# Kernel optimization log

Measured on AMD Instinct MI355X. Metric: run time of the kernel, lower is better.

The kernel has to match this reference:

```python
import jax, jax.numpy as jnp
import numpy as np

B, N, DIM, H, KVAL = 16, 1024, 128, 8, 4  # b divisible by K*K=16; mask batch = B//(K*K)=1


def setup_inputs() -> dict:
    key = jax.random.key(0)
    ks = jax.random.split(key, 6)
    x = jax.random.normal(ks[0], (B, N, DIM), jnp.float32)
    mask = (jax.random.uniform(ks[1], (B // (KVAL * KVAL), N - 1)) < 0.9).astype(jnp.float32)
    maps = (jax.random.uniform(ks[2], (B, N - 1)) < 0.9).astype(jnp.float32)
    Wqkv = jax.random.normal(ks[3], (DIM, 3 * DIM), jnp.float32) / np.sqrt(DIM)
    Wout = jax.random.normal(ks[4], (DIM, DIM), jnp.float32) / np.sqrt(DIM)
    bout = jnp.zeros((DIM,), jnp.float32)
    return {"x": x, "mask": mask, "maps": maps, "Wqkv": Wqkv, "Wout": Wout,
            "bout": bout, "K": KVAL}


def reference(x, mask, maps, Wqkv, Wout, bout, K):
    b, n, dim = x.shape
    h = H
    d = dim // h
    scale = dim ** -0.5
    qkv = x @ Wqkv                                  # [b, n, 3*dim]
    q, k, v = jnp.split(qkv, 3, axis=-1)

    def to_heads(t):
        return t.reshape(b, n, h, d).transpose(0, 2, 1, 3)  # [b, h, n, d]

    q, k, v = to_heads(q), to_heads(k), to_heads(v)
    dots = jnp.einsum('bhid,bhjd->bhij', q, k) * scale      # [b, h, n, n]
    mask_value = -jnp.finfo(dots.dtype).max

    # block mask: pad first key position with 1, broadcast over K*K batch block
    kk = K * K
    m = jnp.pad(mask, ((0, 0), (1, 0)), constant_values=1.0)  # [b//kk, n]
    dots = dots.reshape(b // kk, kk, h, n, n)
    m5 = m[:, None, None, None, :]
    dots = dots * m5 + mask_value * (1.0 - m5)
    dots = dots.reshape(b, h, n, n)

    # map mask: boolean fill per batch element
    mp = jnp.pad(maps, ((0, 0), (1, 0)), constant_values=1.0)  # [b, n]
    dots = jnp.where(mp[:, None, None, :] != 0, dots, mask_value)

    attn = jax.nn.softmax(dots, axis=-1)
    out = jnp.einsum('bhij,bhjd->bhid', attn, v)            # [b, h, n, d]
    out = out.transpose(0, 2, 1, 3).reshape(b, n, dim)      # [b, n, dim]
    return out @ Wout + bout
```

## Files before the change

### kernel.cpp

```cpp
#include <hip/hip_runtime.h>
#include <math.h>

#define B_   16
#define N_   1024
#define DIM_ 128
#define H_   8
#define D_   16
#define BH_  128

typedef unsigned short u16;
typedef unsigned int   u32;
typedef __attribute__((ext_vector_type(8))) short short8;
typedef __attribute__((ext_vector_type(4))) float f32x4;

__device__ __forceinline__ float bf2f(u16 u) {
    union { u32 i; float f; } c; c.i = ((u32)u) << 16; return c.f;
}
__device__ __forceinline__ u16 f2bf(float f) {
    union { float f; u32 i; } c; c.f = f;
    u32 r = c.i + 0x7FFFu + ((c.i >> 16) & 1u);
    return (u16)(r >> 16);
}
__device__ __forceinline__ u32 pack2bf(float a, float b) {
    union { float f; u32 i; } ca, cb; ca.f = a; cb.f = b;
    return ((ca.i + 0x8000u) >> 16) | ((cb.i + 0x8000u) & 0xFFFF0000u);
}
union frag8 { short8 s; u32 w[4]; };

#define BF_ONE  ((short)0x3F80)
#define BF_NINF ((u16)0xFF80)

#define SCALE_L2E (0.08838834764831845f * 1.4426950408889634f)

__global__ __launch_bounds__(256) void prep_kernel(
    const float* __restrict__ x, const float* __restrict__ Wqkv,
    const float* __restrict__ Wout,
    u16* __restrict__ xb, u16* __restrict__ wqkvb, u16* __restrict__ woutb)
{
    const int b = blockIdx.x, tid = threadIdx.x;
    if (b < 2048) {
        const int i = b * 256 + tid;
        float4 v = ((const float4*)x)[i];
        ushort4 o = make_ushort4(f2bf(v.x), f2bf(v.y), f2bf(v.z), f2bf(v.w));
        *(ushort4*)(xb + (size_t)i * 4) = o;
    } else {
        const int t = (b - 2048) * 256 + tid;
        if (t < 49152) {
            const int k = t / 384, col = t - k * 384;
            wqkvb[(size_t)col * 128 + k] = f2bf(Wqkv[t]);
        } else {
            const int t2 = t - 49152;
            const int k = t2 >> 7, col = t2 & 127;
            woutb[(size_t)col * 128 + k] = f2bf(Wout[t2]);
        }
    }
}

__global__ __launch_bounds__(256) void qkv_kernel(
    const u16* __restrict__ xb, const u16* __restrict__ wqkvb,
    const float* __restrict__ maskp, const float* __restrict__ mapsp,
    u16* __restrict__ qws, u16* __restrict__ kws2, u16* __restrict__ vtws)
{
    const int tid  = threadIdx.x;
    const int wave = tid >> 6, lane = tid & 63;
    const int i16  = lane & 15, quad = lane >> 4;
    const int cb   = blockIdx.x % 6;
    const int rb   = blockIdx.x / 6;
    const int row_m = rb * 64 + wave * 16;

    const u16* xp = xb + (size_t)(row_m + i16) * 128;
    const u16* wb = wqkvb + (size_t)(cb * 64 + i16) * 128;

    f32x4 acc0 = {0,0,0,0}, acc1 = {0,0,0,0}, acc2 = {0,0,0,0}, acc3 = {0,0,0,0};

    #pragma unroll
    for (int ks = 0; ks < 4; ks++) {
        const int k0 = ks * 32 + quad * 8;
        const short8 a = *(const short8*)(xp + k0);
        acc0 = __builtin_amdgcn_mfma_f32_16x16x32_bf16(
                   a, *(const short8*)(wb + k0), acc0, 0, 0, 0);
        acc1 = __builtin_amdgcn_mfma_f32_16x16x32_bf16(
                   a, *(const short8*)(wb + 16 * 128 + k0), acc1, 0, 0, 0);
        acc2 = __builtin_amdgcn_mfma_f32_16x16x32_bf16(
                   a, *(const short8*)(wb + 32 * 128 + k0), acc2, 0, 0, 0);
        acc3 = __builtin_amdgcn_mfma_f32_16x16x32_bf16(
                   a, *(const short8*)(wb + 48 * 128 + k0), acc3, 0, 0, 0);
    }

    const int which = (cb * 64) >> 7;
    const int row   = row_m + quad * 4;
    const int bb    = row >> 10, n = row & 1023;

    #define STORE_CT(CT, ACC) { \
        const int c  = (cb * 64 + CT * 16) & 127; \
        const int h  = c >> 4; \
        const int bh = bb * 8 + h; \
        const int dd = i16; \
        if (which == 0) { \
            u16* p = qws + ((size_t)(bh * N_ + n)) * 16 + dd; \
            p[0]  = f2bf(ACC[0] * SCALE_L2E); p[16] = f2bf(ACC[1] * SCALE_L2E); \
            p[32] = f2bf(ACC[2] * SCALE_L2E); p[48] = f2bf(ACC[3] * SCALE_L2E); \
        } else if (which == 1) { \
            u16* p = kws2 + ((size_t)(bh * N_ + n)) * 32 + dd; \
            p[0]  = f2bf(ACC[0]); p[32] = f2bf(ACC[1]); \
            p[64] = f2bf(ACC[2]); p[96] = f2bf(ACC[3]); \
            if (dd == 0) { \
                _Pragma("unroll") \
                for (int r = 0; r < 4; r++) { \
                    const int nr = n + r; \
                    const bool valid = (nr == 0) || \
                        (maskp[nr - 1] != 0.0f && mapsp[bb * (N_ - 1) + nr - 1] != 0.0f); \
                    kws2[((size_t)(bh * N_ + nr)) * 32 + 16] = valid ? (u16)0 : BF_NINF; \
                } \
            } \
        } else { \
            *(ushort4*)(vtws + ((size_t)(bh * 16 + dd)) * N_ + n) = \
                make_ushort4(f2bf(ACC[0]), f2bf(ACC[1]), f2bf(ACC[2]), f2bf(ACC[3])); \
        } }
    STORE_CT(0, acc0)
    STORE_CT(1, acc1)
    STORE_CT(2, acc2)
    STORE_CT(3, acc3)
    #undef STORE_CT
}

__global__ __launch_bounds__(256) void attn_kernel(
    const u16* __restrict__ qws, const u16* __restrict__ kws2, const u16* __restrict__ vtws,
    u16* __restrict__ attn)
{
    const int tid  = threadIdx.x;
    const int wave = tid >> 6, lane = tid & 63;
    const int i16  = lane & 15, quad = lane >> 4;
    const int bh   = blockIdx.x;
    const int qb   = blockIdx.y;
    const int bb   = bh >> 3, h = bh & 7;
    const int qrow0 = qb * 256 + wave * 64;
    const int perm = ((i16 & 12) << 1) | (i16 & 3);

    const short8 zero8 = {0,0,0,0,0,0,0,0};
    const short8 ones8 = {BF_ONE,BF_ONE,BF_ONE,BF_ONE,BF_ONE,BF_ONE,BF_ONE,BF_ONE};

    short8 qf0 = zero8, qf1 = zero8, qf2 = zero8, qf3 = zero8;
    if (lane < 32) {
        const u16* qp = qws + ((size_t)(bh * N_ + qrow0 + i16)) * 16 + quad * 8;
        qf0 = *(const short8*)(qp);
        qf1 = *(const short8*)(qp + 256);
        qf2 = *(const short8*)(qp + 512);
        qf3 = *(const short8*)(qp + 768);
    } else if (lane < 48) {
        qf0[0] = BF_ONE; qf1[0] = BF_ONE; qf2[0] = BF_ONE; qf3[0] = BF_ONE;
    }

    const u16* kpA = kws2 + ((size_t)(bh * N_ + perm)) * 32 + quad * 8;
    const u16* kpB = kpA + 4 * 32;
    const u16* vp  = vtws + ((size_t)(bh * 16 + i16)) * N_ + quad * 8;

    f32x4 o0 = {0,0,0,0}, o1 = {0,0,0,0}, o2 = {0,0,0,0}, o3 = {0,0,0,0};
    f32x4 l0 = {0,0,0,0}, l1 = {0,0,0,0}, l2 = {0,0,0,0}, l3 = {0,0,0,0};
    const f32x4 zc = {0.f, 0.f, 0.f, 0.f};

    #pragma unroll 2
    for (int j0 = 0; j0 < N_; j0 += 32) {
        const short8 kfA = *(const short8*)kpA;
        const short8 kfB = *(const short8*)kpB;
        const short8 vf  = *(const short8*)vp;
        kpA += 32 * 32; kpB += 32 * 32; vp += 32;

        #define TILE(QF, O, L) { \
            f32x4 stA = __builtin_amdgcn_mfma_f32_16x16x32_bf16(kfA, QF, zc, 0, 0, 0); \
            f32x4 stB = __builtin_amdgcn_mfma_f32_16x16x32_bf16(kfB, QF, zc, 0, 0, 0); \
            float pA0 = __builtin_amdgcn_exp2f(stA[0]); \
            float pA1 = __builtin_amdgcn_exp2f(stA[1]); \
            float pA2 = __builtin_amdgcn_exp2f(stA[2]); \
            float pA3 = __builtin_amdgcn_exp2f(stA[3]); \
            float pB0 = __builtin_amdgcn_exp2f(stB[0]); \
            float pB1 = __builtin_amdgcn_exp2f(stB[1]); \
            float pB2 = __builtin_amdgcn_exp2f(stB[2]); \
            float pB3 = __builtin_amdgcn_exp2f(stB[3]); \
            frag8 pk; \
            pk.w[0] = pack2bf(pA0, pA1); pk.w[1] = pack2bf(pA2, pA3); \
            pk.w[2] = pack2bf(pB0, pB1); pk.w[3] = pack2bf(pB2, pB3); \
            O = __builtin_amdgcn_mfma_f32_16x16x32_bf16(vf,    pk.s, O, 0, 0, 0); \
            L = __builtin_amdgcn_mfma_f32_16x16x32_bf16(ones8, pk.s, L, 0, 0, 0); \
        }
        TILE(qf0, o0, l0)
        TILE(qf1, o1, l1)
        TILE(qf2, o2, l2)
        TILE(qf3, o3, l3)
        #undef TILE
    }

    #define OUT_T(T, O, L) { \
        const float inv = 1.0f / L[0]; \
        ushort4 pko = make_ushort4(f2bf(O[0] * inv), f2bf(O[1] * inv), \
                                   f2bf(O[2] * inv), f2bf(O[3] * inv)); \
        *(ushort4*)(attn + ((size_t)(bb * N_ + qrow0 + T * 16 + i16)) * DIM_ \
                    + h * 16 + quad * 4) = pko; }
    OUT_T(0, o0, l0)
    OUT_T(1, o1, l1)
    OUT_T(2, o2, l2)
    OUT_T(3, o3, l3)
    #undef OUT_T
}

__global__ __launch_bounds__(256) void out_kernel(
    const u16* __restrict__ attnw, const u16* __restrict__ woutb,
    const float* __restrict__ boutp, float* __restrict__ outp)
{
    const int tid  = threadIdx.x;
    const int wave = tid >> 6, lane = tid & 63;
    const int i16  = lane & 15, quad = lane >> 4;
    const int cb   = blockIdx.x & 1;
    const int rb   = blockIdx.x >> 1;
    const int row_m = rb * 64 + wave * 16;

    const u16* ap = attnw + (size_t)(row_m + i16) * 128;
    const u16* wb = woutb + (size_t)(cb * 64 + i16) * 128;

    f32x4 acc0 = {0,0,0,0}, acc1 = {0,0,0,0}, acc2 = {0,0,0,0}, acc3 = {0,0,0,0};

    #pragma unroll
    for (int ks = 0; ks < 4; ks++) {
        const int k0 = ks * 32 + quad * 8;
        const short8 a = *(const short8*)(ap + k0);
        acc0 = __builtin_amdgcn_mfma_f32_16x16x32_bf16(
                   a, *(const short8*)(wb + k0), acc0, 0, 0, 0);
        acc1 = __builtin_amdgcn_mfma_f32_16x16x32_bf16(
                   a, *(const short8*)(wb + 16 * 128 + k0), acc1, 0, 0, 0);
        acc2 = __builtin_amdgcn_mfma_f32_16x16x32_bf16(
                   a, *(const short8*)(wb + 32 * 128 + k0), acc2, 0, 0, 0);
        acc3 = __builtin_amdgcn_mfma_f32_16x16x32_bf16(
                   a, *(const short8*)(wb + 48 * 128 + k0), acc3, 0, 0, 0);
    }

    const int row = row_m + quad * 4;
    #define STORE_CT(CT, ACC) { \
        const int col = cb * 64 + CT * 16 + i16; \
        const float bo = boutp[col]; \
        float* op = outp + (size_t)row * 128 + col; \
        op[0 * 128] = ACC[0] + bo; \
        op[1 * 128] = ACC[1] + bo; \
        op[2 * 128] = ACC[2] + bo; \
        op[3 * 128] = ACC[3] + bo; \
    }
    STORE_CT(0, acc0)
    STORE_CT(1, acc1)
    STORE_CT(2, acc2)
    STORE_CT(3, acc3)
    #undef STORE_CT
}

extern "C" void kernel_launch(void* const* d_in, const int* in_sizes, int n_in,
                              void* d_out, int out_size, void* d_ws, size_t ws_size,
                              hipStream_t stream) {
    const float* x    = (const float*)d_in[0];
    const float* mask = (const float*)d_in[1];
    const float* maps = (const float*)d_in[2];
    const float* Wqkv = (const float*)d_in[3];
    const float* Wout = (const float*)d_in[4];
    const float* bout = (const float*)d_in[5];
    u16* qws    = (u16*)d_ws;
    u16* kws2   = qws   + (size_t)2 * 1024 * 1024;
    u16* vtws   = kws2  + (size_t)4 * 1024 * 1024;
    u16* attn   = vtws  + (size_t)2 * 1024 * 1024;
    u16* xbws   = attn  + (size_t)2 * 1024 * 1024;
    u16* wqkvb  = xbws  + (size_t)2 * 1024 * 1024;
    u16* woutb  = wqkvb + (size_t)384 * 128;

    prep_kernel<<<dim3(2304), dim3(256), 0, stream>>>(x, Wqkv, Wout, xbws, wqkvb, woutb);
    qkv_kernel<<<dim3(1536), dim3(256), 0, stream>>>(xbws, wqkvb, mask, maps, qws, kws2, vtws);
    attn_kernel<<<dim3(128, 4), dim3(256), 0, stream>>>(qws, kws2, vtws, attn);
    out_kernel<<<dim3(512), dim3(256), 0, stream>>>(attn, woutb, bout, (float*)d_out);
}
```

Baseline: 134.9 us.

## Fuse all four stages into one cooperative kernel with grid syncs

Replaces the four separate launches (weight/x conversion, QKV projection, attention, output projection) with a single cooperative kernel of 512 blocks that uses grid.sync between stages. The QKV stage now converts x from fp32 to bf16 in registers instead of running a separate conversion pass, and each block covers three column tiles. This targets launch overhead and the round trip of writing and rereading bf16 x. In exchange the grid is fixed at 512 blocks for every stage, which lowers parallelism in the QKV stage, and the grid-wide barriers add cost. The old four-kernel path remains as a fallback if the cooperative launch fails.

```diff
diff --git a/kernel.cpp b/kernel.cpp
--- a/kernel.cpp
+++ b/kernel.cpp
@@ -1,5 +1,8 @@
 #include <hip/hip_runtime.h>
+#include <hip/hip_cooperative_groups.h>
 #include <math.h>
+
+namespace cg = cooperative_groups;
 
 #define B_   16
 #define N_   1024
@@ -29,8 +32,216 @@
 
 #define BF_ONE  ((short)0x3F80)
 #define BF_NINF ((u16)0xFF80)
-
 #define SCALE_L2E (0.08838834764831845f * 1.4426950408889634f)
+
+#define MFMA16 __builtin_amdgcn_mfma_f32_16x16x32_bf16
+
+__global__ __launch_bounds__(256) void fused_kernel(
+    const float* __restrict__ x, const float* __restrict__ maskp,
+    const float* __restrict__ mapsp, const float* __restrict__ Wqkv,
+    const float* __restrict__ Wout, const float* __restrict__ boutp,
+    u16* __restrict__ qws, u16* __restrict__ kws2, u16* __restrict__ vtws,
+    u16* __restrict__ attnw, u16* __restrict__ wqkvb, u16* __restrict__ woutb,
+    float* __restrict__ outp)
+{
+    cg::grid_group grid = cg::this_grid();
+    const int blk  = blockIdx.x;
+    const int tid  = threadIdx.x;
+    const int wave = tid >> 6, lane = tid & 63;
+    const int i16  = lane & 15, quad = lane >> 4;
+
+    {
+        const int t = blk * 256 + tid;
+        if (t < 49152) {
+            const int k = t / 384, col = t - k * 384;
+            wqkvb[(size_t)col * 128 + k] = f2bf(Wqkv[t]);
+        } else if (t < 65536) {
+            const int t2 = t - 49152;
+            const int k = t2 >> 7, col = t2 & 127;
+            woutb[(size_t)col * 128 + k] = f2bf(Wout[t2]);
+        }
+    }
+    grid.sync();
+
+    {
+        const int rb  = blk >> 1;
+        const int cb0 = (blk & 1) * 3;
+        const int row_m = rb * 64 + wave * 16;
+        const float* xp = x + (size_t)(row_m + i16) * 128;
+
+        short8 a0, a1, a2, a3;
+        #define LOADA(A, K0) { \
+            const int k0 = (K0) + quad * 8; \
+            const float4 xa = *(const float4*)(xp + k0); \
+            const float4 xb2 = *(const float4*)(xp + k0 + 4); \
+            frag8 t_; \
+            t_.w[0] = pack2bf(xa.x, xa.y); t_.w[1] = pack2bf(xa.z, xa.w); \
+            t_.w[2] = pack2bf(xb2.x, xb2.y); t_.w[3] = pack2bf(xb2.z, xb2.w); \
+            A = t_.s; }
+        LOADA(a0, 0) LOADA(a1, 32) LOADA(a2, 64) LOADA(a3, 96)
+        #undef LOADA
+
+        const int row = row_m + quad * 4;
+        const int bb  = row >> 10, n = row & 1023;
+
+        for (int ci = 0; ci < 3; ci++) {
+            const int cb = cb0 + ci;
+            const u16* wb = wqkvb + (size_t)(cb * 64 + i16) * 128;
+            f32x4 acc0 = {0,0,0,0}, acc1 = {0,0,0,0}, acc2 = {0,0,0,0}, acc3 = {0,0,0,0};
+            #define KSTEP(A, K0) { \
+                const int k0 = (K0) + quad * 8; \
+                acc0 = MFMA16(A, *(const short8*)(wb + k0),            acc0, 0,0,0); \
+                acc1 = MFMA16(A, *(const short8*)(wb + 16*128 + k0),   acc1, 0,0,0); \
+                acc2 = MFMA16(A, *(const short8*)(wb + 32*128 + k0),   acc2, 0,0,0); \
+                acc3 = MFMA16(A, *(const short8*)(wb + 48*128 + k0),   acc3, 0,0,0); }
+            KSTEP(a0, 0) KSTEP(a1, 32) KSTEP(a2, 64) KSTEP(a3, 96)
+            #undef KSTEP
+
+            const int which = (cb * 64) >> 7;
+            #define STORE_CT(CT, ACC) { \
+                const int c  = (cb * 64 + CT * 16) & 127; \
+                const int h  = c >> 4; \
+                const int bh = bb * 8 + h; \
+                const int dd = i16; \
+                if (which == 0) { \
+                    u16* p = qws + ((size_t)(bh * N_ + n)) * 16 + dd; \
+                    p[0]  = f2bf(ACC[0] * SCALE_L2E); p[16] = f2bf(ACC[1] * SCALE_L2E); \
+                    p[32] = f2bf(ACC[2] * SCALE_L2E); p[48] = f2bf(ACC[3] * SCALE_L2E); \
+                } else if (which == 1) { \
+                    u16* p = kws2 + ((size_t)(bh * N_ + n)) * 32 + dd; \
+                    p[0]  = f2bf(ACC[0]); p[32] = f2bf(ACC[1]); \
+                    p[64] = f2bf(ACC[2]); p[96] = f2bf(ACC[3]); \
+                    if (dd == 0) { \
+                        _Pragma("unroll") \
+                        for (int r = 0; r < 4; r++) { \
+                            const int nr = n + r; \
+                            const bool valid = (nr == 0) || \
+                                (maskp[nr - 1] != 0.0f && mapsp[bb * (N_ - 1) + nr - 1] != 0.0f); \
+                            kws2[((size_t)(bh * N_ + nr)) * 32 + 16] = valid ? (u16)0 : BF_NINF; \
+                        } \
+                    } \
+                } else { \
+                    *(ushort4*)(vtws + ((size_t)(bh * 16 + dd)) * N_ + n) = \
+                        make_ushort4(f2bf(ACC[0]), f2bf(ACC[1]), f2bf(ACC[2]), f2bf(ACC[3])); \
+                } }
+            STORE_CT(0, acc0)
+            STORE_CT(1, acc1)
+            STORE_CT(2, acc2)
+            STORE_CT(3, acc3)
+            #undef STORE_CT
+        }
+    }
+    grid.sync();
+
+    {
+        const int bh = blk >> 2;
+        const int qb = blk & 3;
+        const int bb = bh >> 3, h = bh & 7;
+        const int qrow0 = qb * 256 + wave * 64;
+        const int perm = ((i16 & 12) << 1) | (i16 & 3);
+
+        const short8 zero8 = {0,0,0,0,0,0,0,0};
+        const short8 ones8 = {BF_ONE,BF_ONE,BF_ONE,BF_ONE,BF_ONE,BF_ONE,BF_ONE,BF_ONE};
+
+        short8 qf0 = zero8, qf1 = zero8, qf2 = zero8, qf3 = zero8;
+        if (lane < 32) {
+            const u16* qp = qws + ((size_t)(bh * N_ + qrow0 + i16)) * 16 + quad * 8;
+            qf0 = *(const short8*)(qp);
+            qf1 = *(const short8*)(qp + 256);
+            qf2 = *(const short8*)(qp + 512);
+            qf3 = *(const short8*)(qp + 768);
+        } else if (lane < 48) {
+            qf0[0] = BF_ONE; qf1[0] = BF_ONE; qf2[0] = BF_ONE; qf3[0] = BF_ONE;
+        }
+
+        const u16* kpA = kws2 + ((size_t)(bh * N_ + perm)) * 32 + quad * 8;
+        const u16* kpB = kpA + 4 * 32;
+        const u16* vp  = vtws + ((size_t)(bh * 16 + i16)) * N_ + quad * 8;
+
+        f32x4 o0 = {0,0,0,0}, o1 = {0,0,0,0}, o2 = {0,0,0,0}, o3 = {0,0,0,0};
+        f32x4 l0 = {0,0,0,0}, l1 = {0,0,0,0}, l2 = {0,0,0,0}, l3 = {0,0,0,0};
+        const f32x4 zc = {0.f, 0.f, 0.f, 0.f};
+
+        #pragma unroll 2
+        for (int j0 = 0; j0 < N_; j0 += 32) {
+            const short8 kfA = *(const short8*)kpA;
+            const short8 kfB = *(const short8*)kpB;
+            const short8 vf  = *(const short8*)vp;
+            kpA += 32 * 32; kpB += 32 * 32; vp += 32;
+
+            #define TILE(QF, O, L) { \
+                f32x4 stA = MFMA16(kfA, QF, zc, 0, 0, 0); \
+                f32x4 stB = MFMA16(kfB, QF, zc, 0, 0, 0); \
+                float pA0 = __builtin_amdgcn_exp2f(stA[0]); \
+                float pA1 = __builtin_amdgcn_exp2f(stA[1]); \
+                float pA2 = __builtin_amdgcn_exp2f(stA[2]); \
+                float pA3 = __builtin_amdgcn_exp2f(stA[3]); \
+                float pB0 = __builtin_amdgcn_exp2f(stB[0]); \
+                float pB1 = __builtin_amdgcn_exp2f(stB[1]); \
+                float pB2 = __builtin_amdgcn_exp2f(stB[2]); \
+                float pB3 = __builtin_amdgcn_exp2f(stB[3]); \
+                frag8 pk; \
+                pk.w[0] = pack2bf(pA0, pA1); pk.w[1] = pack2bf(pA2, pA3); \
+                pk.w[2] = pack2bf(pB0, pB1); pk.w[3] = pack2bf(pB2, pB3); \
+                O = MFMA16(vf,    pk.s, O, 0, 0, 0); \
+                L = MFMA16(ones8, pk.s, L, 0, 0, 0); }
+            TILE(qf0, o0, l0)
+            TILE(qf1, o1, l1)
+            TILE(qf2, o2, l2)
+            TILE(qf3, o3, l3)
+            #undef TILE
+        }
+
+        #define OUT_T(T, O, L) { \
+            const float inv = 1.0f / L[0]; \
+            ushort4 pko = make_ushort4(f2bf(O[0] * inv), f2bf(O[1] * inv), \
+                                       f2bf(O[2] * inv), f2bf(O[3] * inv)); \
+            *(ushort4*)(attnw + ((size_t)(bb * N_ + qrow0 + T * 16 + i16)) * DIM_ \
+                        + h * 16 + quad * 4) = pko; }
+        OUT_T(0, o0, l0)
+        OUT_T(1, o1, l1)
+        OUT_T(2, o2, l2)
+        OUT_T(3, o3, l3)
+        #undef OUT_T
+    }
+    grid.sync();
+
+    {
+        const int cb = blk & 1;
+        const int rb = blk >> 1;
+        const int row_m = rb * 64 + wave * 16;
+
+        const u16* ap = attnw + (size_t)(row_m + i16) * 128;
+        const u16* wb = woutb + (size_t)(cb * 64 + i16) * 128;
+
+        f32x4 acc0 = {0,0,0,0}, acc1 = {0,0,0,0}, acc2 = {0,0,0,0}, acc3 = {0,0,0,0};
+
+        #pragma unroll
+        for (int ks = 0; ks < 4; ks++) {
+            const int k0 = ks * 32 + quad * 8;
+            const short8 a = *(const short8*)(ap + k0);
+            acc0 = MFMA16(a, *(const short8*)(wb + k0),          acc0, 0, 0, 0);
+            acc1 = MFMA16(a, *(const short8*)(wb + 16*128 + k0), acc1, 0, 0, 0);
+            acc2 = MFMA16(a, *(const short8*)(wb + 32*128 + k0), acc2, 0, 0, 0);
+            acc3 = MFMA16(a, *(const short8*)(wb + 48*128 + k0), acc3, 0, 0, 0);
+        }
+
+        const int row = row_m + quad * 4;
+        #define STORE_CT(CT, ACC) { \
+            const int col = cb * 64 + CT * 16 + i16; \
+            const float bo = boutp[col]; \
+            float* op = outp + (size_t)row * 128 + col; \
+            op[0 * 128] = ACC[0] + bo; \
+            op[1 * 128] = ACC[1] + bo; \
+            op[2 * 128] = ACC[2] + bo; \
+            op[3 * 128] = ACC[3] + bo; }
+        STORE_CT(0, acc0)
+        STORE_CT(1, acc1)
+        STORE_CT(2, acc2)
+        STORE_CT(3, acc3)
+        #undef STORE_CT
+    }
+}
 
 __global__ __launch_bounds__(256) void prep_kernel(
     const float* __restrict__ x, const float* __restrict__ Wqkv,
@@ -77,14 +288,10 @@
     for (int ks = 0; ks < 4; ks++) {
         const int k0 = ks * 32 + quad * 8;
         const short8 a = *(const short8*)(xp + k0);
-        acc0 = __builtin_amdgcn_mfma_f32_16x16x32_bf16(
-                   a, *(const short8*)(wb + k0), acc0, 0, 0, 0);
-        acc1 = __builtin_amdgcn_mfma_f32_16x16x32_bf16(
-                   a, *(const short8*)(wb + 16 * 128 + k0), acc1, 0, 0, 0);
-        acc2 = __builtin_amdgcn_mfma_f32_16x16x32_bf16(
-                   a, *(const short8*)(wb + 32 * 128 + k0), acc2, 0, 0, 0);
-        acc3 = __builtin_amdgcn_mfma_f32_16x16x32_bf16(
-                   a, *(const short8*)(wb + 48 * 128 + k0), acc3, 0, 0, 0);
+        acc0 = MFMA16(a, *(const short8*)(wb + k0),          acc0, 0, 0, 0);
+        acc1 = MFMA16(a, *(const short8*)(wb + 16*128 + k0), acc1, 0, 0, 0);
+        acc2 = MFMA16(a, *(const short8*)(wb + 32*128 + k0), acc2, 0, 0, 0);
+        acc3 = MFMA16(a, *(const short8*)(wb + 48*128 + k0), acc3, 0, 0, 0);
     }
 
     const int which = (cb * 64) >> 7;
@@ -167,8 +374,8 @@
         kpA += 32 * 32; kpB += 32 * 32; vp += 32;
 
         #define TILE(QF, O, L) { \
-            f32x4 stA = __builtin_amdgcn_mfma_f32_16x16x32_bf16(kfA, QF, zc, 0, 0, 0); \
-            f32x4 stB = __builtin_amdgcn_mfma_f32_16x16x32_bf16(kfB, QF, zc, 0, 0, 0); \
+            f32x4 stA = MFMA16(kfA, QF, zc, 0, 0, 0); \
+            f32x4 stB = MFMA16(kfB, QF, zc, 0, 0, 0); \
             float pA0 = __builtin_amdgcn_exp2f(stA[0]); \
             float pA1 = __builtin_amdgcn_exp2f(stA[1]); \
             float pA2 = __builtin_amdgcn_exp2f(stA[2]); \
@@ -180,9 +387,8 @@
             frag8 pk; \
             pk.w[0] = pack2bf(pA0, pA1); pk.w[1] = pack2bf(pA2, pA3); \
             pk.w[2] = pack2bf(pB0, pB1); pk.w[3] = pack2bf(pB2, pB3); \
-            O = __builtin_amdgcn_mfma_f32_16x16x32_bf16(vf,    pk.s, O, 0, 0, 0); \
-            L = __builtin_amdgcn_mfma_f32_16x16x32_bf16(ones8, pk.s, L, 0, 0, 0); \
-        }
+            O = MFMA16(vf,    pk.s, O, 0, 0, 0); \
+            L = MFMA16(ones8, pk.s, L, 0, 0, 0); }
         TILE(qf0, o0, l0)
         TILE(qf1, o1, l1)
         TILE(qf2, o2, l2)
@@ -223,14 +429,10 @@
     for (int ks = 0; ks < 4; ks++) {
         const int k0 = ks * 32 + quad * 8;
         const short8 a = *(const short8*)(ap + k0);
-        acc0 = __builtin_amdgcn_mfma_f32_16x16x32_bf16(
-                   a, *(const short8*)(wb + k0), acc0, 0, 0, 0);
-        acc1 = __builtin_amdgcn_mfma_f32_16x16x32_bf16(
-                   a, *(const short8*)(wb + 16 * 128 + k0), acc1, 0, 0, 0);
-        acc2 = __builtin_amdgcn_mfma_f32_16x16x32_bf16(
-                   a, *(const short8*)(wb + 32 * 128 + k0), acc2, 0, 0, 0);
-        acc3 = __builtin_amdgcn_mfma_f32_16x16x32_bf16(
-                   a, *(const short8*)(wb + 48 * 128 + k0), acc3, 0, 0, 0);
+        acc0 = MFMA16(a, *(const short8*)(wb + k0),          acc0, 0, 0, 0);
+        acc1 = MFMA16(a, *(const short8*)(wb + 16*128 + k0), acc1, 0, 0, 0);
+        acc2 = MFMA16(a, *(const short8*)(wb + 32*128 + k0), acc2, 0, 0, 0);
+        acc3 = MFMA16(a, *(const short8*)(wb + 48*128 + k0), acc3, 0, 0, 0);
     }
 
     const int row = row_m + quad * 4;
@@ -241,8 +443,7 @@
         op[0 * 128] = ACC[0] + bo; \
         op[1 * 128] = ACC[1] + bo; \
         op[2 * 128] = ACC[2] + bo; \
-        op[3 * 128] = ACC[3] + bo; \
-    }
+        op[3 * 128] = ACC[3] + bo; }
     STORE_CT(0, acc0)
     STORE_CT(1, acc1)
     STORE_CT(2, acc2)
@@ -262,13 +463,24 @@
     u16* qws    = (u16*)d_ws;
     u16* kws2   = qws   + (size_t)2 * 1024 * 1024;
     u16* vtws   = kws2  + (size_t)4 * 1024 * 1024;
-    u16* attn   = vtws  + (size_t)2 * 1024 * 1024;
-    u16* xbws   = attn  + (size_t)2 * 1024 * 1024;
-    u16* wqkvb  = xbws  + (size_t)2 * 1024 * 1024;
+    u16* attnw  = vtws  + (size_t)2 * 1024 * 1024;
+    u16* wqkvb  = attnw + (size_t)2 * 1024 * 1024;
     u16* woutb  = wqkvb + (size_t)384 * 128;
-
-    prep_kernel<<<dim3(2304), dim3(256), 0, stream>>>(x, Wqkv, Wout, xbws, wqkvb, woutb);
-    qkv_kernel<<<dim3(1536), dim3(256), 0, stream>>>(xbws, wqkvb, mask, maps, qws, kws2, vtws);
-    attn_kernel<<<dim3(128, 4), dim3(256), 0, stream>>>(qws, kws2, vtws, attn);
-    out_kernel<<<dim3(512), dim3(256), 0, stream>>>(attn, woutb, bout, (float*)d_out);
-}
+    u16* xbws   = woutb + (size_t)128 * 128;
+    float* outp = (float*)d_out;
+
+    void* args[] = { (void*)&x, (void*)&mask, (void*)&maps, (void*)&Wqkv,
+                     (void*)&Wout, (void*)&bout, (void*)&qws, (void*)&kws2,
+                     (void*)&vtws, (void*)&attnw, (void*)&wqkvb, (void*)&woutb,
+                     (void*)&outp };
+    hipError_t err = hipLaunchCooperativeKernel(
+        reinterpret_cast<const void*>(fused_kernel),
+        dim3(512), dim3(256), args, 0, stream);
+
+    if (err != hipSuccess) {
+        prep_kernel<<<dim3(2304), dim3(256), 0, stream>>>(x, Wqkv, Wout, xbws, wqkvb, woutb);
+        qkv_kernel<<<dim3(1536), dim3(256), 0, stream>>>(xbws, wqkvb, mask, maps, qws, kws2, vtws);
+        attn_kernel<<<dim3(128, 4), dim3(256), 0, stream>>>(qws, kws2, vtws, attnw);
+        out_kernel<<<dim3(512), dim3(256), 0, stream>>>(attnw, woutb, bout, outp);
+    }
+}
```

Result: slower. 291.6 us (+116.1%).
